# Kernel optimization log

Hardware: AMD Instinct MI355X
Metric: run time of the kernel (lower is better)

Reference implementation:

```python
import jax, jax.numpy as jnp
import numpy as np

SCALE = float(1 << 15)
PREEMPH = 0.97
FRAME_LEN = 400
FRAME_SHIFT = 160
FFT_SIZE = 512
N_RFFT = FFT_SIZE // 2 + 1  # 257
EPS = float(np.finfo(np.float32).eps)


def _mel_scale(f):
    return 1127.0 * np.log(1.0 + f / 700.0)


def _get_mel_banks(num_bins=80, window_length_padded=512, sample_freq=16000.0,
                   low_freq=20.0, high_freq=0.0):
    # Kaldi-style triangular mel banks (vtln_warp=1.0 -> no warp)
    num_fft_bins = window_length_padded // 2  # 256
    nyquist = 0.5 * sample_freq
    if high_freq <= 0.0:
        high_freq = nyquist + high_freq  # 8000.0
    fft_bin_width = sample_freq / window_length_padded
    mel_low = _mel_scale(low_freq)
    mel_high = _mel_scale(high_freq)
    mel_delta = (mel_high - mel_low) / (num_bins + 1)
    bins = np.arange(num_bins, dtype=np.float64)[:, None]
    left = mel_low + bins * mel_delta
    center = left + mel_delta
    right = center + mel_delta
    mel_freqs = _mel_scale(fft_bin_width * np.arange(num_fft_bins, dtype=np.float64))[None, :]
    up = (mel_freqs - left) / (center - left)
    down = (right - mel_freqs) / (right - center)
    banks = np.maximum(0.0, np.minimum(up, down))  # [80, 256]
    return banks.astype(np.float32)


def _buffers():
    # Hamming window, periodic=False: 0.54 - 0.46*cos(2*pi*n/(N-1))
    n = np.arange(FRAME_LEN, dtype=np.float64)
    window = (0.54 - 0.46 * np.cos(2.0 * np.pi * n / (FRAME_LEN - 1))).astype(np.float32)
    mel = _get_mel_banks()  # [80, 256]
    mel_padded = np.pad(mel, ((0, 0), (0, 1)))  # pad one zero column -> [80, 257]
    mel_filters = mel_padded.T.copy()  # [257, 80]
    k = np.arange(N_RFFT, dtype=np.float64)
    t = np.arange(FFT_SIZE, dtype=np.float64)
    angles = 2.0 * np.pi * k[:, None] * t[None, :] / FFT_SIZE
    dft_cos = np.cos(angles).astype(np.float32)  # [257, 512]
    dft_sin = np.sin(angles).astype(np.float32)  # [257, 512]
    return window, mel_filters, dft_cos, dft_sin


def setup_inputs() -> dict:
    key = jax.random.key(0)
    waveforms = jax.random.normal(key, (32, 1, 480000), dtype=jnp.float32)
    window, mel_filters, dft_cos, dft_sin = _buffers()
    return {
        "waveforms": waveforms,
        "window": jnp.asarray(window),
        "mel_filters": jnp.asarray(mel_filters),
        "dft_cos": jnp.asarray(dft_cos),
        "dft_sin": jnp.asarray(dft_sin),
    }


def reference(waveforms, window, mel_filters, dft_cos, dft_sin):
    signal = waveforms[:, 0, :] * SCALE  # [B, T]
    T = signal.shape[-1]
    n_frames = (T - FRAME_LEN) // FRAME_SHIFT + 1
    # strided framing (equivalent to conv1d with identity kernel, stride=160)
    idx = jnp.arange(n_frames)[:, None] * FRAME_SHIFT + jnp.arange(FRAME_LEN)[None, :]
    frames = signal[:, idx]  # [B, F, 400]
    frames = frames - jnp.mean(frames, axis=2, keepdims=True)
    # pre-emphasis with replicate-padded previous sample
    prev = jnp.concatenate([frames[..., :1], frames[..., :-1]], axis=-1)
    frames = (frames - PREEMPH * prev) * window  # windowing fused
    frames = jnp.pad(frames, ((0, 0), (0, 0), (0, FFT_SIZE - FRAME_LEN)))  # [B, F, 512]
    real = jnp.matmul(frames, dft_cos.T)  # [B, F, 257]
    imag = jnp.matmul(frames, dft_sin.T)
    spectrum = real * real + imag * imag  # power spectrum
    mel = jnp.matmul(spectrum, mel_filters)  # [B, F, 80]
    mel = jnp.log(jnp.maximum(mel, EPS))
    return mel - jnp.mean(mel, axis=1, keepdims=True)
```

## Files before the change

### kernel.cpp

```cpp
#include <hip/hip_runtime.h>

#define BATCH     32
#define T_SAMP    480000
#define NFRAMES   2998
#define KLEN      400
#define KF        256
#define NMEL      80
#define EPS_F     1.1920928955078125e-07f
#define SCALE2    1073741824.0f
#define SPLIT_S   2048.0f
#define SPLIT_INV 4.8828125e-4f
#define MTE       132
#define NPART     16

typedef _Float16 f16x8 __attribute__((ext_vector_type(8)));
typedef float    f32x4 __attribute__((ext_vector_type(4)));

__global__ __launch_bounds__(256) void FbankWrapper_14285061226526_kernel(float* mpart)
{
    int i = blockIdx.x * 256 + threadIdx.x;
    if (i < NPART * BATCH * NMEL) mpart[i] = 0.f;
}

__global__ __launch_bounds__(256) void k_prep(const float* __restrict__ melf,
                                              const float* __restrict__ dcos,
                                              const float* __restrict__ dsin,
                                              int* __restrict__ loE, int* __restrict__ hiE,
                                              int* __restrict__ loO, int* __restrict__ hiO,
                                              float* __restrict__ melfTe,
                                              float* __restrict__ melfTo,
                                              _Float16* __restrict__ Bhe, _Float16* __restrict__ Ble,
                                              _Float16* __restrict__ Bho, _Float16* __restrict__ Blo)
{
    const int bid = blockIdx.x;
    const int tid = threadIdx.x;

    if (bid < 80) {
        __shared__ int sE0, sE1, sO0, sO1;
        if (tid == 0) { sE0 = 999; sE1 = 0; sO0 = 999; sO1 = 0; }
        __syncthreads();
        const int m = bid;
        if (tid < 129) {
            int bin = (tid == 0) ? 0 : (tid == 128) ? 256 : 2 * tid;
            float w = melf[(size_t)bin * NMEL + m];
            melfTe[(size_t)m * MTE + tid] = w;
            if (w > 0.f) { atomicMin(&sE0, tid); atomicMax(&sE1, tid + 1); }
        }
        if (tid < 128) {
            float w = melf[(size_t)(2 * tid + 1) * NMEL + m];
            melfTo[(size_t)m * MTE + tid] = w;
            if (w > 0.f) { atomicMin(&sO0, tid); atomicMax(&sO1, tid + 1); }
        }
        if (tid == 0) {
            melfTe[(size_t)m * MTE + 129] = 0.f;
            melfTe[(size_t)m * MTE + 130] = 0.f;
            melfTe[(size_t)m * MTE + 131] = 0.f;
            melfTo[(size_t)m * MTE + 128] = 0.f;
            melfTo[(size_t)m * MTE + 129] = 0.f;
            melfTo[(size_t)m * MTE + 130] = 0.f;
            melfTo[(size_t)m * MTE + 131] = 0.f;
        }
        __syncthreads();
        if (tid == 0) { loE[m] = sE0; hiE[m] = sE1; loO[m] = sO0; hiO[m] = sO1; }
        return;
    }

    int id = (bid - 80) * 256 + tid;
    if (id >= 16384) return;
    int g  = id >> 13;
    int r  = id & 8191;
    int ch = r >> 8;
    int c  = r & 255;
    int k  = ch * 8;
    int bin; int sn;
    if (g == 0) { bin = (c == 0) ? 0 : (c == 1) ? 256 : 2 * (c >> 1); sn = (c >= 2) && (c & 1); }
    else        { bin = 2 * (c >> 1) + 1;                             sn = c & 1; }
    const float* src = (sn ? dsin : dcos) + (size_t)bin * 512 + k;
    f16x8 hv, lv;
    #pragma unroll
    for (int j = 0; j < 8; ++j) {
        float v = src[j];
        _Float16 h = (_Float16)v;
        hv[j] = h;
        lv[j] = (_Float16)((v - (float)h) * SPLIT_S);
    }
    size_t off = ((size_t)ch * 256 + c) * 8;
    *(f16x8*)((g ? Bho : Bhe) + off) = hv;
    *(f16x8*)((g ? Blo : Ble) + off) = lv;
}

__device__ inline void y8_compute(const float* __restrict__ sig,
                                  const float* __restrict__ window,
                                  int k0, float mean, float ys[8])
{
    float4 x0 = *(const float4*)(sig + k0);
    float4 x1 = *(const float4*)(sig + k0 + 4);
    float4 w0 = *(const float4*)(window + k0);
    float4 w1 = *(const float4*)(window + k0 + 4);
    float xm1 = (k0 > 0) ? sig[k0 - 1] : x0.x;
    float xs[8] = {x0.x, x0.y, x0.z, x0.w, x1.x, x1.y, x1.z, x1.w};
    float wv[8] = {w0.x, w0.y, w0.z, w0.w, w1.x, w1.y, w1.z, w1.w};
    #pragma unroll
    for (int j = 0; j < 8; ++j) {
        float xp = (j == 0) ? xm1 : xs[j - 1];
        ys[j] = (xs[j] - 0.97f * xp - 0.03f * mean) * wv[j];
    }
}

__device__ inline void split_store(_Float16* dh, _Float16* dl, const float ys[8])
{
    f16x8 hv, lv;
    #pragma unroll
    for (int j = 0; j < 8; ++j) {
        _Float16 h = (_Float16)ys[j];
        hv[j] = h;
        lv[j] = (_Float16)((ys[j] - (float)h) * SPLIT_S);
    }
    *(f16x8*)dh = hv;
    *(f16x8*)dl = lv;
}

__global__ __launch_bounds__(512, 4) void k_main_pre(const float* __restrict__ wav,
                                                     const float* __restrict__ window,
                                                     const float* __restrict__ melfTe,
                                                     const float* __restrict__ melfTo,
                                                     const int* __restrict__ loE,
                                                     const int* __restrict__ hiE,
                                                     const int* __restrict__ loO,
                                                     const int* __restrict__ hiO,
                                                     const _Float16* __restrict__ Bhe,
                                                     const _Float16* __restrict__ Ble,
                                                     const _Float16* __restrict__ Bho,
                                                     const _Float16* __restrict__ Blo,
                                                     float* __restrict__ out,
                                                     float* __restrict__ mpart)
{
    __shared__ __align__(16) _Float16 Aeh[32][264];
    __shared__ __align__(16) _Float16 Ael[32][264];
    __shared__ __align__(16) _Float16 Aoh[32][168];
    __shared__ __align__(16) _Float16 Aol[32][168];
    __shared__ __align__(16) float    Sp[32][132];

    const int tid  = threadIdx.x;
    const int lane = tid & 63;
    const int wid  = tid >> 6;
    const int tile = blockIdx.x;

    {
        int fr = tid >> 4, og = tid & 15;
        int fb = tile * 32 + fr;
        int b  = fb / NFRAMES;
        int f  = fb - b * NFRAMES;
        const float* sig = wav + (size_t)b * T_SAMP + (size_t)f * 160;

        float s = 0.f;
        #pragma unroll
        for (int i = 0; i < 4; ++i) {
            int k0 = og * 8 + 128 * i;
            if (k0 < KLEN) {
                float4 x0 = *(const float4*)(sig + k0);
                float4 x1 = *(const float4*)(sig + k0 + 4);
                s += x0.x + x0.y + x0.z + x0.w + x1.x + x1.y + x1.z + x1.w;
            }
        }
        s += __shfl_xor(s, 1);
        s += __shfl_xor(s, 2);
        s += __shfl_xor(s, 4);
        s += __shfl_xor(s, 8);
        float mean = s * (1.0f / (float)KLEN);

        #pragma unroll
        for (int t2 = 0; t2 < 2; ++t2) {
            int c  = og + 16 * t2;
            int k0 = c * 8;
            float ys[8];
            y8_compute(sig, window, k0, mean, ys);
            if (c < 18) {
                float yb[8], ye[8], yo[8];
                y8_compute(sig, window, k0 + 256, mean, yb);
                #pragma unroll
                for (int j = 0; j < 8; ++j) { ye[j] = ys[j] + yb[j]; yo[j] = ys[j] - yb[j]; }
                split_store(&Aeh[fr][k0], &Ael[fr][k0], ye);
                split_store(&Aoh[fr][k0], &Aol[fr][k0], yo);
            } else {
                split_store(&Aeh[fr][k0], &Ael[fr][k0], ys);
                if (k0 < 160)
                    split_store(&Aoh[fr][k0], &Aol[fr][k0], ys);
            }
        }
    }
    __syncthreads();

    const int q  = lane >> 4, lr = lane & 15;
    const int mf = tid & 31;
    const int mg = tid >> 5;

    float accm[5];
    #pragma unroll
    for (int t = 0; t < 5; ++t) accm[t] = 0.f;

    #pragma unroll
    for (int p = 0; p < 2; ++p) {
        f32x4 aM[2][2], aC[2][2];
        #pragma unroll
        for (int mt = 0; mt < 2; ++mt)
            #pragma unroll
            for (int nt = 0; nt < 2; ++nt) {
                aM[mt][nt] = (f32x4){0.f, 0.f, 0.f, 0.f};
                aC[mt][nt] = (f32x4){0.f, 0.f, 0.f, 0.f};
            }

        const _Float16* Bh_ = p ? Bho : Bhe;
        const _Float16* Bl_ = p ? Blo : Ble;
        const _Float16* bph[2];
        const _Float16* blp[2];
        #pragma unroll
        for (int nt = 0; nt < 2; ++nt) {
            int c = wid * 32 + nt * 16 + lr;
            size_t off = (size_t)q * 2048 + (size_t)c * 8;
            bph[nt] = Bh_ + off;
            blp[nt] = Bl_ + off;
        }

        #pragma unroll
        for (int s = 0; s < 8; ++s) {
            const int kk = s * 32;
            f16x8 ah[2], al[2], bh[2], bl[2];
            if (p == 0 || s >= 5) {
                #pragma unroll
                for (int mt = 0; mt < 2; ++mt) {
                    ah[mt] = *(const f16x8*)&Aeh[mt * 16 + lr][kk + q * 8];
                    al[mt] = *(const f16x8*)&Ael[mt * 16 + lr][kk + q * 8];
                }
            } else {
                #pragma unroll
                for (int mt = 0; mt < 2; ++mt) {
                    ah[mt] = *(const f16x8*)&Aoh[mt * 16 + lr][kk + q * 8];
                    al[mt] = *(const f16x8*)&Aol[mt * 16 + lr][kk + q * 8];
                }
            }
            #pragma unroll
            for (int nt = 0; nt < 2; ++nt) {
                bh[nt] = *(const f16x8*)(bph[nt] + (size_t)s * 8192);
                bl[nt] = *(const f16x8*)(blp[nt] + (size_t)s * 8192);
            }
            __builtin_amdgcn_s_setprio(1);
            #pragma unroll
            for (int mt = 0; mt < 2; ++mt)
                #pragma unroll
                for (int nt = 0; nt < 2; ++nt)
                    aM[mt][nt] = __builtin_amdgcn_mfma_f32_16x16x32_f16(
                        ah[mt], bh[nt], aM[mt][nt], 0, 0, 0);
            #pragma unroll
            for (int mt = 0; mt < 2; ++mt)
                #pragma unroll
                for (int nt = 0; nt < 2; ++nt)
                    aC[mt][nt] = __builtin_amdgcn_mfma_f32_16x16x32_f16(
                        al[mt], bh[nt], aC[mt][nt], 0, 0, 0);
            #pragma unroll
            for (int mt = 0; mt < 2; ++mt)
                #pragma unroll
                for (int nt = 0; nt < 2; ++nt)
                    aC[mt][nt] = __builtin_amdgcn_mfma_f32_16x16x32_f16(
                        ah[mt], bl[nt], aC[mt][nt], 0, 0, 0);
            __builtin_amdgcn_s_setprio(0);
        }

        __syncthreads();
        #pragma unroll
        for (int mt = 0; mt < 2; ++mt)
            #pragma unroll
            for (int nt = 0; nt < 2; ++nt)
                #pragma unroll
                for (int r = 0; r < 4; ++r) {
                    float v = aM[mt][nt][r] + aC[mt][nt][r] * SPLIT_INV;
                    float o = __shfl_xor(v, 1);
                    int row = mt * 16 + q * 4 + r;
                    if (p == 0 && wid == 0 && nt == 0 && lr < 2) {
                        if (lr == 0) Sp[row][0] = v * v;
                    } else if ((lane & 1) == 0) {
                        int slot = (wid * 32 + nt * 16 + lr) >> 1;
                        Sp[row][slot] = v * v + o * o;
                    }
                }
        __syncthreads();

        const float* mfT = p ? melfTo : melfTe;
        const int*   loP = p ? loO : loE;
        const int*   hiP = p ? hiO : hiE;
        #pragma unroll
        for (int t = 0; t < 5; ++t) {
            int m  = mg + 16 * t;
            int ks = loP[m], ke = hiP[m];
            const float* wrow = mfT + (size_t)m * MTE;
            for (int k4 = ks & ~3; k4 < ke; k4 += 4) {
                f32x4  sv = *(const f32x4*)&Sp[mf][k4];
                float4 wv = *(const float4*)(wrow + k4);
                accm[t] += sv[0] * wv.x + sv[1] * wv.y + sv[2] * wv.z + sv[3] * wv.w;
            }
        }
    }

    {
        int fb = tile * 32 + mf;
        int b  = fb / NFRAMES;
        int b0 = (tile * 32) / NFRAMES;
        int bL = (tile * 32 + 31) / NFRAMES;
        size_t row = (size_t)fb;
        float* mp = mpart + (size_t)(tile & (NPART - 1)) * (BATCH * NMEL);
        float lg[5];
        #pragma unroll
        for (int t = 0; t < 5; ++t) {
            lg[t] = logf(fmaxf(accm[t] * SCALE2, EPS_F));
            out[row * NMEL + mg + 16 * t] = lg[t];
        }
        if (bL == b0) {
            #pragma unroll
            for (int t = 0; t < 5; ++t) {
                float v = lg[t];
                #pragma unroll
                for (int d = 1; d < 32; d <<= 1) v += __shfl_xor(v, d);
                if (mf == 0)
                    atomicAdd(&mp[b0 * NMEL + mg + 16 * t], v);
            }
        } else {
            #pragma unroll
            for (int t = 0; t < 5; ++t) {
                float v0 = (b == b0) ? lg[t] : 0.f;
                float v1 = lg[t] - v0;
                #pragma unroll
                for (int d = 1; d < 32; d <<= 1) {
                    v0 += __shfl_xor(v0, d);
                    v1 += __shfl_xor(v1, d);
                }
                if (mf == 0) {
                    atomicAdd(&mp[b0 * NMEL + mg + 16 * t], v0);
                    atomicAdd(&mp[bL * NMEL + mg + 16 * t], v1);
                }
            }
        }
    }
}

__global__ __launch_bounds__(256) void k_norm(const float* __restrict__ mpart,
                                              float* __restrict__ out)
{
    __shared__ float lmean[NMEL];
    const int PER = NFRAMES * NMEL;
    const int b   = blockIdx.y;
    const int tid = threadIdx.x;
    if (tid < NMEL) {
        float s = 0.f;
        #pragma unroll
        for (int p = 0; p < NPART; ++p)
            s += mpart[(size_t)p * (BATCH * NMEL) + b * NMEL + tid];
        lmean[tid] = s * (1.0f / (float)NFRAMES);
    }
    __syncthreads();
    int e0 = blockIdx.x * 1024 + tid;
    #pragma unroll
    for (int j = 0; j < 4; ++j) {
        int e = e0 + j * 256;
        if (e < PER) {
            int m = e % NMEL;
            size_t idx = (size_t)b * PER + e;
            out[idx] = out[idx] - lmean[m];
        }
    }
}

extern "C" void kernel_launch(void* const* d_in, const int* in_sizes, int n_in,
                              void* d_out, int out_size, void* d_ws, size_t ws_size,
                              hipStream_t stream)
{
    const float* wav    = (const float*)d_in[0];
    const float* window = (const float*)d_in[1];
    const float* melf   = (const float*)d_in[2];
    const float* dcos   = (const float*)d_in[3];
    const float* dsin   = (const float*)d_in[4];
    float* out = (float*)d_out;

    char* ws = (char*)d_ws;
    int*       loE    = (int*)(ws + 10240);
    int*       hiE    = (int*)(ws + 10560);
    int*       loO    = (int*)(ws + 10880);
    int*       hiO    = (int*)(ws + 11200);
    float*     melfTe = (float*)(ws + 11520);
    float*     melfTo = (float*)(ws + 53760);
    _Float16*  Bhe    = (_Float16*)(ws + 96256);
    _Float16*  Ble    = (_Float16*)(ws + 227328);
    _Float16*  Bho    = (_Float16*)(ws + 358400);
    _Float16*  Blo    = (_Float16*)(ws + 489472);
    float*     mpart  = (float*)(ws + 620544);

    FbankWrapper_14285061226526_kernel<<<160, 256, 0, stream>>>(mpart);
    k_prep<<<144, 256, 0, stream>>>(melf, dcos, dsin, loE, hiE, loO, hiO,
                                    melfTe, melfTo, Bhe, Ble, Bho, Blo);
    k_main_pre<<<2998, 512, 0, stream>>>(wav, window, melfTe, melfTo,
                                         loE, hiE, loO, hiO,
                                         Bhe, Ble, Bho, Blo, out, mpart);
    k_norm<<<dim3((NFRAMES * NMEL + 1023) / 1024, BATCH), 256, 0, stream>>>(mpart, out);
}
```

Baseline: 255.2 us.

## Alias odd-half and spectrum LDS buffers, swap pass order, raise occupancy

```diff
diff --git a/kernel.cpp b/kernel.cpp
--- a/kernel.cpp
+++ b/kernel.cpp
@@ -120,7 +120,7 @@
     *(f16x8*)dl = lv;
 }
 
-__global__ __launch_bounds__(512, 4) void k_main_pre(const float* __restrict__ wav,
+__global__ __launch_bounds__(512, 6) void k_main_pre(const float* __restrict__ wav,
                                                      const float* __restrict__ window,
                                                      const float* __restrict__ melfTe,
                                                      const float* __restrict__ melfTo,
@@ -137,9 +137,10 @@
 {
     __shared__ __align__(16) _Float16 Aeh[32][264];
     __shared__ __align__(16) _Float16 Ael[32][264];
-    __shared__ __align__(16) _Float16 Aoh[32][168];
-    __shared__ __align__(16) _Float16 Aol[32][168];
-    __shared__ __align__(16) float    Sp[32][132];
+    __shared__ __align__(16) char     ux[32 * 152 * 4];
+    _Float16 (*Aoh)[152] = (_Float16(*)[152])ux;
+    _Float16 (*Aol)[152] = (_Float16(*)[152])(ux + 9728);
+    float    (*Sp)[132]  = (float(*)[132])ux;
 
     const int tid  = threadIdx.x;
     const int lane = tid & 63;
@@ -184,8 +185,6 @@
                 split_store(&Aoh[fr][k0], &Aol[fr][k0], yo);
             } else {
                 split_store(&Aeh[fr][k0], &Ael[fr][k0], ys);
-                if (k0 < 160)
-                    split_store(&Aoh[fr][k0], &Aol[fr][k0], ys);
             }
         }
     }
@@ -210,8 +209,8 @@
                 aC[mt][nt] = (f32x4){0.f, 0.f, 0.f, 0.f};
             }
 
-        const _Float16* Bh_ = p ? Bho : Bhe;
-        const _Float16* Bl_ = p ? Blo : Ble;
+        const _Float16* Bh_ = p ? Bhe : Bho;
+        const _Float16* Bl_ = p ? Ble : Blo;
         const _Float16* bph[2];
         const _Float16* blp[2];
         #pragma unroll
@@ -226,25 +225,21 @@
         for (int s = 0; s < 8; ++s) {
             const int kk = s * 32;
             f16x8 ah[2], al[2], bh[2], bl[2];
-            if (p == 0 || s >= 5) {
-                #pragma unroll
-                for (int mt = 0; mt < 2; ++mt) {
-                    ah[mt] = *(const f16x8*)&Aeh[mt * 16 + lr][kk + q * 8];
-                    al[mt] = *(const f16x8*)&Ael[mt * 16 + lr][kk + q * 8];
-                }
-            } else {
-                #pragma unroll
-                for (int mt = 0; mt < 2; ++mt) {
-                    ah[mt] = *(const f16x8*)&Aoh[mt * 16 + lr][kk + q * 8];
-                    al[mt] = *(const f16x8*)&Aol[mt * 16 + lr][kk + q * 8];
-                }
+            const bool useAo = (p == 0) && (kk + q * 8 < 144);
+            #pragma unroll
+            for (int mt = 0; mt < 2; ++mt) {
+                const _Float16* ph = useAo ? &Aoh[mt * 16 + lr][kk + q * 8]
+                                           : &Aeh[mt * 16 + lr][kk + q * 8];
+                const _Float16* pl = useAo ? &Aol[mt * 16 + lr][kk + q * 8]
+                                           : &Ael[mt * 16 + lr][kk + q * 8];
+                ah[mt] = *(const f16x8*)ph;
+                al[mt] = *(const f16x8*)pl;
             }
             #pragma unroll
             for (int nt = 0; nt < 2; ++nt) {
                 bh[nt] = *(const f16x8*)(bph[nt] + (size_t)s * 8192);
                 bl[nt] = *(const f16x8*)(blp[nt] + (size_t)s * 8192);
             }
-            __builtin_amdgcn_s_setprio(1);
             #pragma unroll
             for (int mt = 0; mt < 2; ++mt)
                 #pragma unroll
@@ -263,7 +258,6 @@
                 for (int nt = 0; nt < 2; ++nt)
                     aC[mt][nt] = __builtin_amdgcn_mfma_f32_16x16x32_f16(
                         ah[mt], bl[nt], aC[mt][nt], 0, 0, 0);
-            __builtin_amdgcn_s_setprio(0);
         }
 
         __syncthreads();
@@ -276,7 +270,7 @@
                     float v = aM[mt][nt][r] + aC[mt][nt][r] * SPLIT_INV;
                     float o = __shfl_xor(v, 1);
                     int row = mt * 16 + q * 4 + r;
-                    if (p == 0 && wid == 0 && nt == 0 && lr < 2) {
+                    if (p == 1 && wid == 0 && nt == 0 && lr < 2) {
                         if (lr == 0) Sp[row][0] = v * v;
                     } else if ((lane & 1) == 0) {
                         int slot = (wid * 32 + nt * 16 + lr) >> 1;
@@ -285,9 +279,9 @@
                 }
         __syncthreads();
 
-        const float* mfT = p ? melfTo : melfTe;
-        const int*   loP = p ? loO : loE;
-        const int*   hiP = p ? hiO : hiE;
+        const float* mfT = p ? melfTe : melfTo;
+        const int*   loP = p ? loE : loO;
+        const int*   hiP = p ? hiE : hiO;
         #pragma unroll
         for (int t = 0; t < 5; ++t) {
             int m  = mg + 16 * t;
```

New measurement: 267.1 us. 1.05x slower.
